# Optimization experiments

Measured on AMD Instinct MI355X. Metric: run time of the kernel, lower is better.

Reference implementation:

```python
import jax, jax.numpy as jnp
import numpy as np

B, N, CHUNK, LAH = 2, 16, 60, 4
EXT = CHUNK + LAH            # extended chunk size C+R
S = N * EXT                  # flattened (chunked) time dim
D, FF, H, K, L = 512, 2048, 8, 31, 6
DH = D // H
EPS = 1e-5


def _ln(x, g, b):
    m = x.mean(-1, keepdims=True)
    v = ((x - m) ** 2).mean(-1, keepdims=True)
    return (x - m) * jax.lax.rsqrt(v + EPS) * g + b


def _chunk_mask(lookahead_size):
    # True = query may attend key. Queries see all past chunks (excluding the
    # carried-over lookahead frames of past chunks) plus the full current
    # extended chunk (its own real frames and its own lookahead frames).
    idx = jnp.arange(S)
    c = idx // EXT           # chunk index of each flattened position
    w = idx % EXT            # position within extended chunk
    past = (c[None, :] < c[:, None]) & (w[None, :] < EXT - lookahead_size)
    curr = c[None, :] == c[:, None]
    return past | curr       # [S, S]


def setup_inputs():
    key = jax.random.key(0)
    ks = iter(jax.random.split(key, 16))

    def pr(shape, s=0.02):
        return jax.random.normal(next(ks), (L,) + shape, jnp.float32) * s

    ones = lambda shape: jnp.ones((L,) + shape, jnp.float32)
    zeros = lambda shape: jnp.zeros((L,) + shape, jnp.float32)
    return dict(
        x=jax.random.normal(next(ks), (B, N, EXT, D), jnp.float32),
        sequence_mask=jnp.ones((B, N, EXT), bool).at[:, -1, CHUNK - 10:].set(False),
        lookahead_size=LAH,
        ff1_lng=ones((D,)), ff1_lnb=zeros((D,)),
        ff1_w1=pr((D, FF)), ff1_b1=zeros((FF,)),
        ff1_w2=pr((FF, D)), ff1_b2=zeros((D,)),
        att_lng=ones((D,)), att_lnb=zeros((D,)),
        wqkv=pr((D, 3 * D)), bqkv=zeros((3 * D,)),
        wo=pr((D, D)), bo=zeros((D,)),
        conv_lng=ones((D,)), conv_lnb=zeros((D,)),
        pw1_w=pr((D, 2 * D)), pw1_b=zeros((2 * D,)),
        dw_w=pr((K, 1, D)), dw_b=zeros((D,)),
        cn_g=ones((D,)), cn_b=zeros((D,)),
        pw2_w=pr((D, D)), pw2_b=zeros((D,)),
        ff2_lng=ones((D,)), ff2_lnb=zeros((D,)),
        ff2_w1=pr((D, FF)), ff2_b1=zeros((FF,)),
        ff2_w2=pr((FF, D)), ff2_b2=zeros((D,)),
        fin_g=ones((D,)), fin_b=zeros((D,)),
    )


def _forward(x, sequence_mask, lookahead_size,
             ff1_lng, ff1_lnb, ff1_w1, ff1_b1, ff1_w2, ff1_b2,
             att_lng, att_lnb, wqkv, bqkv, wo, bo,
             conv_lng, conv_lnb, pw1_w, pw1_b, dw_w, dw_b, cn_g, cn_b, pw2_w, pw2_b,
             ff2_lng, ff2_lnb, ff2_w1, ff2_b1, ff2_w2, ff2_b2, fin_g, fin_b):
    xf = x.reshape(B, S, D)
    key_valid = sequence_mask.reshape(B, S)
    allowed = _chunk_mask(lookahead_size)[None, None] & key_valid[:, None, None, :]  # [B,1,S,S]
    scale = 1.0 / np.sqrt(DH).astype(np.float32)

    def ff(h, lng, lnb, w1, b1, w2, b2):
        h = _ln(h, lng, lnb)
        h = jax.nn.silu(h @ w1 + b1)
        return h @ w2 + b2

    def block(h, pr):
        (f1g, f1b, f1w1, f1b1, f1w2, f1b2,
         alg, alb, wq, bq, wo_, bo_,
         clg, clb, p1w, p1b, dww, dwb, cng, cnb, p2w, p2b,
         f2g, f2b, f2w1, f2b1, f2w2, f2b2, fg, fb) = pr
        # 0.5 * FF1 + residual
        h = 0.5 * ff(h, f1g, f1b, f1w1, f1b1, f1w2, f1b2) + h
        # MHSA with block-diagonal + lookahead chunk mask
        y = _ln(h, alg, alb)
        qkv = y @ wq + bq
        q, k, v = jnp.split(qkv, 3, axis=-1)
        q = q.reshape(B, S, H, DH)
        k = k.reshape(B, S, H, DH)
        v = v.reshape(B, S, H, DH)
        sc = jnp.einsum("bqhd,bkhd->bhqk", q, k) * scale
        sc = jnp.where(allowed, sc, -1e30)
        a = jax.nn.softmax(sc, axis=-1)
        o = jnp.einsum("bhqk,bkhd->bqhd", a, v).reshape(B, S, D)
        h = o @ wo_ + bo_ + h
        # zero padded frames before conv (masked_fill in torch)
        h = jnp.where(key_valid[..., None], h, 0.0)
        # conv module: LN -> pw(2D) -> GLU -> depthwise conv -> LN(NC) -> silu -> pw
        c = _ln(h, clg, clb)
        c = c @ p1w + p1b
        ca, cb = jnp.split(c, 2, axis=-1)
        c = ca * jax.nn.sigmoid(cb)
        c = jax.lax.conv_general_dilated(
            c, dww, window_strides=(1,), padding=[(K // 2, K // 2)],
            dimension_numbers=("NWC", "WIO", "NWC"), feature_group_count=D) + dwb
        c = _ln(c, cng, cnb)
        c = jax.nn.silu(c)
        c = c @ p2w + p2b
        h = c + h
        # 0.5 * FF2 + residual, final LN
        h = 0.5 * ff(h, f2g, f2b, f2w1, f2b1, f2w2, f2b2) + h
        h = _ln(h, fg, fb)
        return h, None

    params = (ff1_lng, ff1_lnb, ff1_w1, ff1_b1, ff1_w2, ff1_b2,
              att_lng, att_lnb, wqkv, bqkv, wo, bo,
              conv_lng, conv_lnb, pw1_w, pw1_b, dw_w, dw_b, cn_g, cn_b, pw2_w, pw2_b,
              ff2_lng, ff2_lnb, ff2_w1, ff2_b1, ff2_w2, ff2_b2, fin_g, fin_b)
    out, _ = jax.lax.scan(block, xf, params)
    # strip lookahead frames: [B, N, C, D]
    return out.reshape(B, N, EXT, D)[:, :, :EXT - lookahead_size]


def reference(x, sequence_mask, lookahead_size,
              ff1_lng, ff1_lnb, ff1_w1, ff1_b1, ff1_w2, ff1_b2,
              att_lng, att_lnb, wqkv, bqkv, wo, bo,
              conv_lng, conv_lnb, pw1_w, pw1_b, dw_w, dw_b, cn_g, cn_b, pw2_w, pw2_b,
              ff2_lng, ff2_lnb, ff2_w1, ff2_b1, ff2_w2, ff2_b2, fin_g, fin_b):
    return _forward(x, sequence_mask, lookahead_size,
                    ff1_lng, ff1_lnb, ff1_w1, ff1_b1, ff1_w2, ff1_b2,
                    att_lng, att_lnb, wqkv, bqkv, wo, bo,
                    conv_lng, conv_lnb, pw1_w, pw1_b, dw_w, dw_b, cn_g, cn_b, pw2_w, pw2_b,
                    ff2_lng, ff2_lnb, ff2_w1, ff2_b1, ff2_w2, ff2_b2, fin_g, fin_b)
```

## Files before the change

### kernel.cpp

```cpp
#include <hip/hip_runtime.h>
#include <hip/hip_bf16.h>
#include <math.h>

#define BB   2
#define NN   16
#define EXTC 64
#define SS   1024
#define DD   512
#define FFD  2048
#define HH   8
#define DHD  64
#define KW   31
#define LL   6
#define BSROWS (BB*SS)
#define LN_EPS 1e-5f

#define EPI_STORE    0
#define EPI_SILU_BF  1
#define EPI_ADD      2
#define EPI_ADDHALF  3
#define EPI_ADD_MASK 4
#define EPI_STORE_BF 5
#define EPI_PART     6

__device__ __forceinline__ int mask_val(const void* m, int i) {
    unsigned int w0 = *(const unsigned int*)m;
    if (w0 == 0x01010101u) return ((const unsigned char*)m)[i];
    if (w0 == 0x3F803F80u) return (((const unsigned short*)m)[i] != 0);
    if (w0 == 0x3F800000u) return (((const float*)m)[i] != 0.0f);
    return (((const int*)m)[i] != 0);
}

__device__ __forceinline__ float sigmoidf_(float x) { return 1.0f / (1.0f + __expf(-x)); }

__device__ __forceinline__ unsigned short f2bf_(float x) {
    unsigned int u = __float_as_uint(x);
    u += 0x7FFF + ((u >> 16) & 1);
    return (unsigned short)(u >> 16);
}

typedef __attribute__((ext_vector_type(8))) short bf16x8;
typedef __attribute__((ext_vector_type(4))) float f32x4;

__global__ __launch_bounds__(256) void ln_kernel(
    const float* __restrict__ in, const float* __restrict__ g,
    const float* __restrict__ b, void* __restrict__ out, int do_silu, int out_bf)
{
    int row = blockIdx.x;
    int t = threadIdx.x;
    const float* ip = in + (size_t)row * DD;
    float v0 = ip[t], v1 = ip[t + 256];
    float s = v0 + v1, ss = v0 * v0 + v1 * v1;
    #pragma unroll
    for (int o = 32; o; o >>= 1) { s += __shfl_down(s, o); ss += __shfl_down(ss, o); }
    __shared__ float sh[8];
    int wid = t >> 6, lane = t & 63;
    if (lane == 0) { sh[wid] = s; sh[4 + wid] = ss; }
    __syncthreads();
    if (t == 0) {
        float S = sh[0] + sh[1] + sh[2] + sh[3];
        float SSum = sh[4] + sh[5] + sh[6] + sh[7];
        float m = S * (1.0f / DD);
        float var = SSum * (1.0f / DD) - m * m;
        sh[0] = m;
        sh[1] = rsqrtf(var + LN_EPS);
    }
    __syncthreads();
    float m = sh[0], rs = sh[1];
    float o0 = (v0 - m) * rs * g[t] + b[t];
    float o1 = (v1 - m) * rs * g[t + 256] + b[t + 256];
    if (do_silu) { o0 = o0 * sigmoidf_(o0); o1 = o1 * sigmoidf_(o1); }
    if (out_bf) {
        unsigned short* op = (unsigned short*)out + (size_t)row * DD;
        op[t] = f2bf_(o0);
        op[t + 256] = f2bf_(o1);
    } else {
        float* op = (float*)out + (size_t)row * DD;
        op[t] = o0;
        op[t + 256] = o1;
    }
}

#define WARENA_LSTRIDE 6029312
__global__ __launch_bounds__(256) void pretrans_kernel(
    const float* __restrict__ w0, const float* __restrict__ w1,
    const float* __restrict__ w2, const float* __restrict__ w3,
    const float* __restrict__ w4, const float* __restrict__ w5,
    const float* __restrict__ w6, const float* __restrict__ w7,
    unsigned short* __restrict__ dst)
{
    const int starts[8] = {0, 256, 512, 704, 768, 896, 960, 1216};
    const int kdim[8]   = {512, 2048, 512, 512, 512, 512, 512, 2048};
    const int ndim[8]   = {2048, 512, 1536, 512, 1024, 512, 2048, 512};
    const int dstoff[8] = {0, 1048576, 2097152, 2883584, 3145728, 3670016, 3932160, 4980736};
    const float* wlist[8] = {w0, w1, w2, w3, w4, w5, w6, w7};
    int layer = blockIdx.y;
    int tile = blockIdx.x;
    int wi = 0;
    #pragma unroll
    for (int i = 7; i >= 1; --i) if (tile >= starts[i]) { wi = i; break; }
    int lt = tile - starts[wi];
    int K = kdim[wi], N = ndim[wi];
    int nT = N >> 6;
    int tk = lt / nT, tn = lt - tk * nT;
    const float* src = wlist[wi] + (size_t)layer * K * N;
    unsigned short* d = dst + (size_t)layer * WARENA_LSTRIDE + dstoff[wi];
    __shared__ float S[64][65];
    int t = threadIdx.x;
    int c = t & 63, r4 = t >> 6;
    #pragma unroll
    for (int u = 0; u < 16; ++u) {
        int row = u * 4 + r4;
        S[row][c] = src[(size_t)(tk * 64 + row) * N + tn * 64 + c];
    }
    __syncthreads();
    #pragma unroll
    for (int u = 0; u < 16; ++u) {
        int nrow = u * 4 + r4;
        d[(size_t)(tn * 64 + nrow) * K + tk * 64 + c] = f2bf_(S[c][nrow]);
    }
}

#define GSTR 72
template<bool WT>
__global__ __launch_bounds__(256) void gemm2_kernel(
    const unsigned short* __restrict__ A, const void* __restrict__ Wv,
    const float* __restrict__ bias, const float* __restrict__ res,
    const void* __restrict__ maskraw,
    float* __restrict__ outf, unsigned short* __restrict__ outb,
    float* __restrict__ part, int M, int N, int Kd, int mode)
{
    __shared__ unsigned short As[64 * GSTR];
    __shared__ unsigned short Bs[64 * GSTR];
    int t = threadIdx.x, lane = t & 63, wave = t >> 6;
    int wr = wave >> 1, wc = wave & 1;
    int l15 = lane & 15, l4 = lane >> 4;
    int row0 = blockIdx.y * 64, col0 = blockIdx.x * 64;
    int kPer = Kd / gridDim.z;
    int k0 = blockIdx.z * kPer;
    int iters = kPer >> 6;
    int ar = t >> 2, ak = (t & 3) * 16;
    int wn = t & 63, wk0 = (t >> 6) * 16;

    f32x4 zero = {0.f, 0.f, 0.f, 0.f};
    f32x4 acc[2][2];
    acc[0][0] = zero; acc[0][1] = zero; acc[1][0] = zero; acc[1][1] = zero;

    uint4 aR0, aR1, wR0, wR1;
    float wF[16];
    {
        const unsigned short* ap = A + (size_t)(row0 + ar) * Kd + k0 + ak;
        aR0 = *(const uint4*)ap; aR1 = *(const uint4*)(ap + 8);
        if constexpr (WT) {
            const unsigned short* wp = (const unsigned short*)Wv + (size_t)(col0 + ar) * Kd + k0 + ak;
            wR0 = *(const uint4*)wp; wR1 = *(const uint4*)(wp + 8);
        } else {
            const float* wp = (const float*)Wv + (size_t)(k0 + wk0) * N + col0 + wn;
            #pragma unroll
            for (int kk = 0; kk < 16; ++kk) wF[kk] = wp[(size_t)kk * N];
        }
    }
    for (int it = 0; it < iters; ++it) {
        __syncthreads();
        *(uint4*)&As[ar * GSTR + ak]     = aR0;
        *(uint4*)&As[ar * GSTR + ak + 8] = aR1;
        if constexpr (WT) {
            *(uint4*)&Bs[ar * GSTR + ak]     = wR0;
            *(uint4*)&Bs[ar * GSTR + ak + 8] = wR1;
        } else {
            union { unsigned short u16[16]; uint4 q[2]; } pk;
            #pragma unroll
            for (int kk = 0; kk < 16; ++kk) pk.u16[kk] = f2bf_(wF[kk]);
            uint4* dstp = (uint4*)&Bs[wn * GSTR + wk0];
            dstp[0] = pk.q[0];
            dstp[1] = pk.q[1];
        }
        __syncthreads();
        if (it + 1 < iters) {
            int kn = k0 + (it + 1) * 64;
            const unsigned short* ap = A + (size_t)(row0 + ar) * Kd + kn + ak;
            aR0 = *(const uint4*)ap; aR1 = *(const uint4*)(ap + 8);
            if constexpr (WT) {
                const unsigned short* wp = (const unsigned short*)Wv + (size_t)(col0 + ar) * Kd + kn + ak;
                wR0 = *(const uint4*)wp; wR1 = *(const uint4*)(wp + 8);
            } else {
                const float* wp = (const float*)Wv + (size_t)(kn + wk0) * N + col0 + wn;
                #pragma unroll
                for (int kk = 0; kk < 16; ++kk) wF[kk] = wp[(size_t)kk * N];
            }
        }
        #pragma unroll
        for (int s = 0; s < 2; ++s) {
            bf16x8 af0 = *(const bf16x8*)&As[(wr * 32 + l15) * GSTR + s * 32 + l4 * 8];
            bf16x8 af1 = *(const bf16x8*)&As[(wr * 32 + 16 + l15) * GSTR + s * 32 + l4 * 8];
            bf16x8 bf0 = *(const bf16x8*)&Bs[(wc * 32 + l15) * GSTR + s * 32 + l4 * 8];
            bf16x8 bf1 = *(const bf16x8*)&Bs[(wc * 32 + 16 + l15) * GSTR + s * 32 + l4 * 8];
            acc[0][0] = __builtin_amdgcn_mfma_f32_16x16x32_bf16(af0, bf0, acc[0][0], 0, 0, 0);
            acc[0][1] = __builtin_amdgcn_mfma_f32_16x16x32_bf16(af0, bf1, acc[0][1], 0, 0, 0);
            acc[1][0] = __builtin_amdgcn_mfma_f32_16x16x32_bf16(af1, bf0, acc[1][0], 0, 0, 0);
            acc[1][1] = __builtin_amdgcn_mfma_f32_16x16x32_bf16(af1, bf1, acc[1][1], 0, 0, 0);
        }
    }
    #pragma unroll
    for (int i = 0; i < 2; i++) {
        #pragma unroll
        for (int j = 0; j < 2; j++) {
            int colb = col0 + wc * 32 + j * 16 + l15;
            #pragma unroll
            for (int r = 0; r < 4; r++) {
                int row = row0 + wr * 32 + i * 16 + l4 * 4 + r;
                size_t off = (size_t)row * N + colb;
                float v = acc[i][j][r];
                if (mode == EPI_PART) { part[(size_t)blockIdx.z * M * N + off] = v; continue; }
                v += bias[colb];
                if (mode == EPI_SILU_BF)       outb[off] = f2bf_(v * sigmoidf_(v));
                else if (mode == EPI_STORE_BF) outb[off] = f2bf_(v);
                else if (mode == EPI_ADD)      outf[off] = v + res[off];
                else if (mode == EPI_ADDHALF)  outf[off] = 0.5f * v + res[off];
                else if (mode == EPI_ADD_MASK) {
                    v = v + res[off];
                    if (!mask_val(maskraw, row)) v = 0.0f;
                    outf[off] = v;
                }
                else                           outf[off] = v;
            }
        }
    }
}

__global__ __launch_bounds__(256) void reduce_addhalf_kernel(
    const float* __restrict__ part, const float* __restrict__ bias,
    float* __restrict__ outAres, int MN, int N)
{
    int idx = (blockIdx.x * 256 + threadIdx.x) * 4;
    float4 p0 = *(const float4*)&part[idx];
    float4 p1 = *(const float4*)&part[MN + idx];
    int col = idx & (N - 1);
    float4 bi = *(const float4*)&bias[col];
    float4 rv = *(const float4*)&outAres[idx];
    float4 o;
    o.x = 0.5f * (p0.x + p1.x + bi.x) + rv.x;
    o.y = 0.5f * (p0.y + p1.y + bi.y) + rv.y;
    o.z = 0.5f * (p0.z + p1.z + bi.z) + rv.z;
    o.w = 0.5f * (p0.w + p1.w + bi.w) + rv.w;
    *(float4*)&outAres[idx] = o;
}

#define QSTR 72
__global__ __launch_bounds__(256) void attn_mfma_kernel(
    const unsigned short* __restrict__ qkv, const void* __restrict__ maskraw,
    const int* __restrict__ lah_ptr, unsigned short* __restrict__ o)
{
    __shared__ unsigned short Qs[64 * QSTR];
    __shared__ unsigned short Ks[64 * QSTR];
    __shared__ unsigned short Vt[64 * QSTR];
    __shared__ unsigned short Ps[64 * QSTR];
    int idx = blockIdx.x;
    int qc = idx & 15;
    int h  = (idx >> 4) & 7;
    int b  = idx >> 7;
    int t  = threadIdx.x;
    int wave = t >> 6, lane = t & 63;
    int l15 = lane & 15, g = lane >> 4;
    int lah = lah_ptr[0];
    int lim = EXTC - lah;
    size_t base = (size_t)b * SS * 3 * DD;
    int ldr = t >> 2;
    int ldc = (t & 3) * 16;

    {
        const unsigned short* gp = qkv + base + (size_t)(qc * 64 + ldr) * (3 * DD) + h * DHD + ldc;
        *(uint4*)&Qs[ldr * QSTR + ldc]     = *(const uint4*)gp;
        *(uint4*)&Qs[ldr * QSTR + ldc + 8] = *(const uint4*)(gp + 8);
    }
    f32x4 accO[4];
    f32x4 zero = {0.f, 0.f, 0.f, 0.f};
    #pragma unroll
    for (int j = 0; j < 4; j++) accO[j] = zero;
    float m[4], l[4];
    #pragma unroll
    for (int r = 0; r < 4; r++) { m[r] = -INFINITY; l[r] = 0.0f; }

    for (int kc = 0; kc <= qc; ++kc) {
        {
            const unsigned short* kp = qkv + base + (size_t)(kc * 64 + ldr) * (3 * DD) + DD + h * DHD + ldc;
            *(uint4*)&Ks[ldr * QSTR + ldc]     = *(const uint4*)kp;
            *(uint4*)&Ks[ldr * QSTR + ldc + 8] = *(const uint4*)(kp + 8);
        }
        {
            const unsigned short* vp = qkv + base + (size_t)(kc * 64 + ldr) * (3 * DD) + 2 * DD + h * DHD + ldc;
            union { uint4 q[2]; unsigned short u16[16]; } vv;
            vv.q[0] = *(const uint4*)vp;
            vv.q[1] = *(const uint4*)(vp + 8);
            #pragma unroll
            for (int u = 0; u < 16; u++)
                Vt[(ldc + u) * QSTR + ldr] = vv.u16[u];
        }
        __syncthreads();
        bf16x8 aq0 = *(const bf16x8*)&Qs[(wave * 16 + l15) * QSTR + g * 8];
        bf16x8 aq1 = *(const bf16x8*)&Qs[(wave * 16 + l15) * QSTR + 32 + g * 8];
        f32x4 sacc[4];
        #pragma unroll
        for (int j = 0; j < 4; j++) {
            bf16x8 bk0 = *(const bf16x8*)&Ks[(j * 16 + l15) * QSTR + g * 8];
            bf16x8 bk1 = *(const bf16x8*)&Ks[(j * 16 + l15) * QSTR + 32 + g * 8];
            sacc[j] = __builtin_amdgcn_mfma_f32_16x16x32_bf16(aq0, bk0, zero, 0, 0, 0);
            sacc[j] = __builtin_amdgcn_mfma_f32_16x16x32_bf16(aq1, bk1, sacc[j], 0, 0, 0);
        }
        bool curr = (kc == qc);
        #pragma unroll
        for (int j = 0; j < 4; ++j) {
            int kpos = j * 16 + l15;
            bool ok = (curr || (kpos < lim)) && (mask_val(maskraw, b * SS + kc * 64 + kpos) != 0);
            #pragma unroll
            for (int r = 0; r < 4; r++)
                sacc[j][r] = ok ? sacc[j][r] * 0.125f : -1e30f;
        }
        #pragma unroll
        for (int r = 0; r < 4; ++r) {
            float rv = fmaxf(fmaxf(sacc[0][r], sacc[1][r]), fmaxf(sacc[2][r], sacc[3][r]));
            rv = fmaxf(rv, __shfl_xor(rv, 1));
            rv = fmaxf(rv, __shfl_xor(rv, 2));
            rv = fmaxf(rv, __shfl_xor(rv, 4));
            rv = fmaxf(rv, __shfl_xor(rv, 8));
            float mn = fmaxf(m[r], rv);
            float alpha = __expf(m[r] - mn);
            float p0 = __expf(sacc[0][r] - mn), p1 = __expf(sacc[1][r] - mn);
            float p2 = __expf(sacc[2][r] - mn), p3 = __expf(sacc[3][r] - mn);
            float ps = p0 + p1 + p2 + p3;
            ps += __shfl_xor(ps, 1);
            ps += __shfl_xor(ps, 2);
            ps += __shfl_xor(ps, 4);
            ps += __shfl_xor(ps, 8);
            l[r] = l[r] * alpha + ps;
            m[r] = mn;
            #pragma unroll
            for (int j = 0; j < 4; j++) accO[j][r] *= alpha;
            int qrow = wave * 16 + g * 4 + r;
            Ps[qrow * QSTR +  0 + l15] = f2bf_(p0);
            Ps[qrow * QSTR + 16 + l15] = f2bf_(p1);
            Ps[qrow * QSTR + 32 + l15] = f2bf_(p2);
            Ps[qrow * QSTR + 48 + l15] = f2bf_(p3);
        }
        __syncthreads();
        bf16x8 ap0 = *(const bf16x8*)&Ps[(wave * 16 + l15) * QSTR + g * 8];
        bf16x8 ap1 = *(const bf16x8*)&Ps[(wave * 16 + l15) * QSTR + 32 + g * 8];
        #pragma unroll
        for (int j = 0; j < 4; j++) {
            bf16x8 bv0 = *(const bf16x8*)&Vt[(j * 16 + l15) * QSTR + g * 8];
            bf16x8 bv1 = *(const bf16x8*)&Vt[(j * 16 + l15) * QSTR + 32 + g * 8];
            accO[j] = __builtin_amdgcn_mfma_f32_16x16x32_bf16(ap0, bv0, accO[j], 0, 0, 0);
            accO[j] = __builtin_amdgcn_mfma_f32_16x16x32_bf16(ap1, bv1, accO[j], 0, 0, 0);
        }
        __syncthreads();
    }
    #pragma unroll
    for (int r = 0; r < 4; r++) {
        float inv = 1.0f / l[r];
        size_t row = (size_t)b * SS + qc * 64 + wave * 16 + g * 4 + r;
        #pragma unroll
        for (int j = 0; j < 4; j++)
            o[row * DD + h * DHD + j * 16 + l15] = f2bf_(accO[j][r] * inv);
    }
}

__global__ __launch_bounds__(256) void glu_kernel(
    const float* __restrict__ in, float* __restrict__ out)
{
    int idx = blockIdx.x * 256 + threadIdx.x;
    int d4 = (idx & 127) * 4;
    int r = idx >> 7;
    float4 a = *(const float4*)&in[(size_t)r * 2 * DD + d4];
    float4 gt = *(const float4*)&in[(size_t)r * 2 * DD + DD + d4];
    float4 res;
    res.x = a.x * sigmoidf_(gt.x);
    res.y = a.y * sigmoidf_(gt.y);
    res.z = a.z * sigmoidf_(gt.z);
    res.w = a.w * sigmoidf_(gt.w);
    *(float4*)&out[(size_t)idx * 4] = res;
}

__global__ __launch_bounds__(256) void dwconv_ln_silu_kernel(
    const float* __restrict__ in, const float* __restrict__ w,
    const float* __restrict__ bias, const float* __restrict__ g,
    const float* __restrict__ be, unsigned short* __restrict__ out)
{
    int t = threadIdx.x;
    int half = t >> 7;
    int row = blockIdx.x * 2 + half;
    int d4 = (t & 127) * 4;
    int s = row & (SS - 1), b = row >> 10;
    float4 acc = *(const float4*)&bias[d4];
    #pragma unroll
    for (int k = 0; k < KW; k++) {
        int sp = s + k - KW / 2;
        if (sp >= 0 && sp < SS) {
            float4 x = *(const float4*)&in[((size_t)b * SS + sp) * DD + d4];
            float4 ww = *(const float4*)&w[k * DD + d4];
            acc.x = fmaf(x.x, ww.x, acc.x);
            acc.y = fmaf(x.y, ww.y, acc.y);
            acc.z = fmaf(x.z, ww.z, acc.z);
            acc.w = fmaf(x.w, ww.w, acc.w);
        }
    }
    float sm = acc.x + acc.y + acc.z + acc.w;
    float sq = acc.x * acc.x + acc.y * acc.y + acc.z * acc.z + acc.w * acc.w;
    #pragma unroll
    for (int o = 32; o; o >>= 1) { sm += __shfl_down(sm, o); sq += __shfl_down(sq, o); }
    __shared__ float sh[8];
    int wid = t >> 6, lane = t & 63;
    if (lane == 0) { sh[wid] = sm; sh[4 + wid] = sq; }
    __syncthreads();
    float S = sh[half * 2] + sh[half * 2 + 1];
    float Q = sh[4 + half * 2] + sh[4 + half * 2 + 1];
    float mean = S * (1.0f / DD);
    float rs = rsqrtf(Q * (1.0f / DD) - mean * mean + LN_EPS);
    float4 gg = *(const float4*)&g[d4];
    float4 bb = *(const float4*)&be[d4];
    float y0 = (acc.x - mean) * rs * gg.x + bb.x;
    float y1 = (acc.y - mean) * rs * gg.y + bb.y;
    float y2 = (acc.z - mean) * rs * gg.z + bb.z;
    float y3 = (acc.w - mean) * rs * gg.w + bb.w;
    y0 *= sigmoidf_(y0); y1 *= sigmoidf_(y1); y2 *= sigmoidf_(y2); y3 *= sigmoidf_(y3);
    uint2 pk;
    pk.x = (unsigned int)f2bf_(y0) | ((unsigned int)f2bf_(y1) << 16);
    pk.y = (unsigned int)f2bf_(y2) | ((unsigned int)f2bf_(y3) << 16);
    *(uint2*)&out[(size_t)row * DD + d4] = pk;
}

__global__ __launch_bounds__(256) void store_out_kernel(
    const float* __restrict__ hbuf, float* __restrict__ out)
{
    int idx = blockIdx.x * 256 + threadIdx.x;
    int d = idx & (DD - 1);
    int rest = idx >> 9;
    int c = rest % 60;
    int bn = rest / 60;
    out[idx] = hbuf[((size_t)bn * EXTC + c) * DD + d];
}

extern "C" void kernel_launch(void* const* d_in, const int* in_sizes, int n_in,
                              void* d_out, int out_size, void* d_ws, size_t ws_size,
                              hipStream_t stream)
{
    const float* x    = (const float*)d_in[0];
    const void*  mask = d_in[1];
    const int*   lah  = (const int*)d_in[2];
    #define P(i) ((const float*)d_in[i])

    char* wsb = (char*)d_ws;
    float*          A   = (float*)(wsb);
    unsigned short* Ybf = (unsigned short*)(wsb + (4u<<20));
    char*           U   = wsb + (6u<<20);
    float*          Db  = (float*)(wsb + (18u<<20));
    unsigned short* Dbf = (unsigned short*)(wsb + (22u<<20));
    float*          Part = (float*)(wsb + (18u<<20));
    float*          Uf  = (float*)U;
    unsigned short* Ub  = (unsigned short*)U;
    unsigned short* Wt  = (unsigned short*)(wsb + (26u<<20));
    bool wt = ws_size >= (100ull << 20);

    hipMemcpyAsync(A, x, (size_t)BSROWS * DD * 4, hipMemcpyDeviceToDevice, stream);
    if (wt) {
        dim3 gpt(1472, LL);
        pretrans_kernel<<<gpt, 256, 0, stream>>>(P(5), P(7), P(11), P(13), P(17),
                                                 P(23), P(27), P(29), Wt);
    }
    const size_t woff[8] = {0, 1048576, 2097152, 2883584, 3145728, 3670016, 3932160, 4980736};

    #define GEMM(grid, Aptr, Wfp, wi, bias, res, mk, of, ob, pt, M_, N_, K_, md)            \
        do { if (wt)                                                                         \
            gemm2_kernel<true><<<grid, 256, 0, stream>>>(Aptr,                               \
                (const void*)(Wt + (size_t)l * WARENA_LSTRIDE + woff[wi]), bias, res, mk,    \
                of, ob, pt, M_, N_, K_, md);                                                 \
        else                                                                                 \
            gemm2_kernel<false><<<grid, 256, 0, stream>>>(Aptr, (const void*)(Wfp), bias,    \
                res, mk, of, ob, pt, M_, N_, K_, md); } while (0)

    dim3 gFF1 (FFD / 64,    BSROWS / 64, 1);
    dim3 gW2  (DD / 64,     BSROWS / 64, 2);
    dim3 gQKV (3 * DD / 64, BSROWS / 64, 1);
    dim3 gP1  (2 * DD / 64, BSROWS / 64, 1);
    dim3 gDx  (DD / 64,     BSROWS / 64, 1);
    int ew4_blocks = BSROWS * DD / 4 / 256;

    for (int l = 0; l < LL; l++) {
        const float* f1g  = P(3)  + (size_t)l * DD;
        const float* f1b  = P(4)  + (size_t)l * DD;
        const float* f1w1 = P(5)  + (size_t)l * DD * FFD;
        const float* f1b1 = P(6)  + (size_t)l * FFD;
        const float* f1w2 = P(7)  + (size_t)l * FFD * DD;
        const float* f1b2 = P(8)  + (size_t)l * DD;
        const float* alg  = P(9)  + (size_t)l * DD;
        const float* alb  = P(10) + (size_t)l * DD;
        const float* wqkv = P(11) + (size_t)l * DD * 3 * DD;
        const float* bqkv = P(12) + (size_t)l * 3 * DD;
        const float* wo   = P(13) + (size_t)l * DD * DD;
        const float* bo   = P(14) + (size_t)l * DD;
        const float* clg  = P(15) + (size_t)l * DD;
        const float* clb  = P(16) + (size_t)l * DD;
        const float* p1w  = P(17) + (size_t)l * DD * 2 * DD;
        const float* p1b  = P(18) + (size_t)l * 2 * DD;
        const float* dww  = P(19) + (size_t)l * KW * DD;
        const float* dwb  = P(20) + (size_t)l * DD;
        const float* cng  = P(21) + (size_t)l * DD;
        const float* cnb  = P(22) + (size_t)l * DD;
        const float* p2w  = P(23) + (size_t)l * DD * DD;
        const float* p2b  = P(24) + (size_t)l * DD;
        const float* f2g  = P(25) + (size_t)l * DD;
        const float* f2b  = P(26) + (size_t)l * DD;
        const float* f2w1 = P(27) + (size_t)l * DD * FFD;
        const float* f2b1 = P(28) + (size_t)l * FFD;
        const float* f2w2 = P(29) + (size_t)l * FFD * DD;
        const float* f2b2 = P(30) + (size_t)l * DD;
        const float* fing = P(31) + (size_t)l * DD;
        const float* finb = P(32) + (size_t)l * DD;

        ln_kernel<<<BSROWS, 256, 0, stream>>>(A, f1g, f1b, Ybf, 0, 1);
        GEMM(gFF1, Ybf, f1w1, 0, f1b1, nullptr, nullptr, nullptr, Ub, nullptr,
             BSROWS, FFD, DD, EPI_SILU_BF);
        GEMM(gW2, Ub, f1w2, 1, nullptr, nullptr, nullptr, nullptr, nullptr, Part,
             BSROWS, DD, FFD, EPI_PART);
        reduce_addhalf_kernel<<<BSROWS * DD / 1024, 256, 0, stream>>>(Part, f1b2, A,
             BSROWS * DD, DD);

        ln_kernel<<<BSROWS, 256, 0, stream>>>(A, alg, alb, Ybf, 0, 1);
        GEMM(gQKV, Ybf, wqkv, 2, bqkv, nullptr, nullptr, nullptr, Ub, nullptr,
             BSROWS, 3 * DD, DD, EPI_STORE_BF);
        attn_mfma_kernel<<<BB * HH * NN, 256, 0, stream>>>(Ub, mask, lah, Dbf);
        GEMM(gDx, Dbf, wo, 3, bo, A, mask, A, nullptr, nullptr,
             BSROWS, DD, DD, EPI_ADD_MASK);

        ln_kernel<<<BSROWS, 256, 0, stream>>>(A, clg, clb, Ybf, 0, 1);
        GEMM(gP1, Ybf, p1w, 4, p1b, nullptr, nullptr, Uf, nullptr, nullptr,
             BSROWS, 2 * DD, DD, EPI_STORE);
        glu_kernel<<<ew4_blocks, 256, 0, stream>>>(Uf, Db);
        dwconv_ln_silu_kernel<<<BSROWS / 2, 256, 0, stream>>>(Db, dww, dwb, cng, cnb, Ybf);
        GEMM(gDx, Ybf, p2w, 5, p2b, A, nullptr, A, nullptr, nullptr,
             BSROWS, DD, DD, EPI_ADD);

        ln_kernel<<<BSROWS, 256, 0, stream>>>(A, f2g, f2b, Ybf, 0, 1);
        GEMM(gFF1, Ybf, f2w1, 6, f2b1, nullptr, nullptr, nullptr, Ub, nullptr,
             BSROWS, FFD, DD, EPI_SILU_BF);
        GEMM(gW2, Ub, f2w2, 7, nullptr, nullptr, nullptr, nullptr, nullptr, Part,
             BSROWS, DD, FFD, EPI_PART);
        reduce_addhalf_kernel<<<BSROWS * DD / 1024, 256, 0, stream>>>(Part, f2b2, A,
             BSROWS * DD, DD);

        ln_kernel<<<BSROWS, 256, 0, stream>>>(A, fing, finb, A, 0, 0);
    }

    store_out_kernel<<<(BB * NN * 60 * DD) / 256, 256, 0, stream>>>(A, (float*)d_out);
    #undef GEMM
    #undef P
}
```

Before: 1.477 ms.

## Fuse split-K reduce with layernorms, fuse pointwise GEMM with GLU, bf16 intermediates

Merges the split-K reduction of each FFN second GEMM with the following layernorm (and, for FFN2, with the final LN, the next layer's first LN and the output strip). Fuses the first conv pointwise GEMM with the GLU gating so it writes bf16 directly and skips the fp32 intermediate. The conv path now stores the GLU output in bf16. Also vectorizes the pretranspose stores and drops the initial memcpy and the separate store kernel. This cuts launches and memory traffic, at the cost of slightly lower precision in the conv intermediate.

```diff
diff --git a/kernel.cpp b/kernel.cpp
--- a/kernel.cpp
+++ b/kernel.cpp
@@ -18,7 +18,6 @@
 #define EPI_STORE    0
 #define EPI_SILU_BF  1
 #define EPI_ADD      2
-#define EPI_ADDHALF  3
 #define EPI_ADD_MASK 4
 #define EPI_STORE_BF 5
 #define EPI_PART     6
@@ -38,13 +37,16 @@
     u += 0x7FFF + ((u >> 16) & 1);
     return (unsigned short)(u >> 16);
 }
+__device__ __forceinline__ float bf2f_(unsigned short b) {
+    return __uint_as_float(((unsigned int)b) << 16);
+}
 
 typedef __attribute__((ext_vector_type(8))) short bf16x8;
 typedef __attribute__((ext_vector_type(4))) float f32x4;
 
 __global__ __launch_bounds__(256) void ln_kernel(
     const float* __restrict__ in, const float* __restrict__ g,
-    const float* __restrict__ b, void* __restrict__ out, int do_silu, int out_bf)
+    const float* __restrict__ b, unsigned short* __restrict__ out)
 {
     int row = blockIdx.x;
     int t = threadIdx.x;
@@ -57,28 +59,91 @@
     int wid = t >> 6, lane = t & 63;
     if (lane == 0) { sh[wid] = s; sh[4 + wid] = ss; }
     __syncthreads();
-    if (t == 0) {
-        float S = sh[0] + sh[1] + sh[2] + sh[3];
-        float SSum = sh[4] + sh[5] + sh[6] + sh[7];
-        float m = S * (1.0f / DD);
-        float var = SSum * (1.0f / DD) - m * m;
-        sh[0] = m;
-        sh[1] = rsqrtf(var + LN_EPS);
-    }
+    float S = sh[0] + sh[1] + sh[2] + sh[3];
+    float Q = sh[4] + sh[5] + sh[6] + sh[7];
+    float m = S * (1.0f / DD);
+    float rs = rsqrtf(Q * (1.0f / DD) - m * m + LN_EPS);
+    out[(size_t)row * DD + t]       = f2bf_((v0 - m) * rs * g[t] + b[t]);
+    out[(size_t)row * DD + t + 256] = f2bf_((v1 - m) * rs * g[t + 256] + b[t + 256]);
+}
+
+__global__ __launch_bounds__(256) void reduce_ln_kernel(
+    const float* __restrict__ part, const float* __restrict__ bias,
+    const float* __restrict__ res, float* __restrict__ A,
+    const float* __restrict__ g, const float* __restrict__ b,
+    unsigned short* __restrict__ Ybf)
+{
+    int row = blockIdx.x, t = threadIdx.x;
+    size_t o0 = (size_t)row * DD + t, o1 = o0 + 256;
+    const int MN = BSROWS * DD;
+    float h0 = 0.5f * (part[o0] + part[MN + o0] + bias[t])       + res[o0];
+    float h1 = 0.5f * (part[o1] + part[MN + o1] + bias[t + 256]) + res[o1];
+    A[o0] = h0; A[o1] = h1;
+    float s = h0 + h1, ss = h0 * h0 + h1 * h1;
+    #pragma unroll
+    for (int o = 32; o; o >>= 1) { s += __shfl_down(s, o); ss += __shfl_down(ss, o); }
+    __shared__ float sh[8];
+    int wid = t >> 6, lane = t & 63;
+    if (lane == 0) { sh[wid] = s; sh[4 + wid] = ss; }
     __syncthreads();
-    float m = sh[0], rs = sh[1];
-    float o0 = (v0 - m) * rs * g[t] + b[t];
-    float o1 = (v1 - m) * rs * g[t + 256] + b[t + 256];
-    if (do_silu) { o0 = o0 * sigmoidf_(o0); o1 = o1 * sigmoidf_(o1); }
-    if (out_bf) {
-        unsigned short* op = (unsigned short*)out + (size_t)row * DD;
-        op[t] = f2bf_(o0);
-        op[t + 256] = f2bf_(o1);
-    } else {
-        float* op = (float*)out + (size_t)row * DD;
-        op[t] = o0;
-        op[t + 256] = o1;
-    }
+    float S = sh[0] + sh[1] + sh[2] + sh[3];
+    float Q = sh[4] + sh[5] + sh[6] + sh[7];
+    float m = S * (1.0f / DD);
+    float rs = rsqrtf(Q * (1.0f / DD) - m * m + LN_EPS);
+    Ybf[o0] = f2bf_((h0 - m) * rs * g[t] + b[t]);
+    Ybf[o1] = f2bf_((h1 - m) * rs * g[t + 256] + b[t + 256]);
+}
+
+__global__ __launch_bounds__(256) void reduce_lnln_kernel(
+    const float* __restrict__ part, const float* __restrict__ bias,
+    float* __restrict__ A,
+    const float* __restrict__ fing, const float* __restrict__ finb,
+    const float* __restrict__ g2, const float* __restrict__ b2,
+    unsigned short* __restrict__ Ybf, int last, float* __restrict__ outp)
+{
+    int row = blockIdx.x, t = threadIdx.x;
+    size_t o0 = (size_t)row * DD + t, o1 = o0 + 256;
+    const int MN = BSROWS * DD;
+    float h0 = 0.5f * (part[o0] + part[MN + o0] + bias[t])       + A[o0];
+    float h1 = 0.5f * (part[o1] + part[MN + o1] + bias[t + 256]) + A[o1];
+    __shared__ float sh[8];
+    int wid = t >> 6, lane = t & 63;
+    {
+        float s = h0 + h1, ss = h0 * h0 + h1 * h1;
+        #pragma unroll
+        for (int o = 32; o; o >>= 1) { s += __shfl_down(s, o); ss += __shfl_down(ss, o); }
+        if (lane == 0) { sh[wid] = s; sh[4 + wid] = ss; }
+    }
+    __syncthreads();
+    float S = sh[0] + sh[1] + sh[2] + sh[3];
+    float Q = sh[4] + sh[5] + sh[6] + sh[7];
+    float m = S * (1.0f / DD);
+    float rs = rsqrtf(Q * (1.0f / DD) - m * m + LN_EPS);
+    float f0 = (h0 - m) * rs * fing[t] + finb[t];
+    float f1 = (h1 - m) * rs * fing[t + 256] + finb[t + 256];
+    A[o0] = f0; A[o1] = f1;
+    if (last) {
+        int c = row & 63, bn = row >> 6;
+        if (c < 60) {
+            size_t oo = ((size_t)(bn * 60 + c)) * DD + t;
+            outp[oo] = f0; outp[oo + 256] = f1;
+        }
+        return;
+    }
+    __syncthreads();
+    {
+        float s = f0 + f1, ss = f0 * f0 + f1 * f1;
+        #pragma unroll
+        for (int o = 32; o; o >>= 1) { s += __shfl_down(s, o); ss += __shfl_down(ss, o); }
+        if (lane == 0) { sh[wid] = s; sh[4 + wid] = ss; }
+    }
+    __syncthreads();
+    float S2 = sh[0] + sh[1] + sh[2] + sh[3];
+    float Q2 = sh[4] + sh[5] + sh[6] + sh[7];
+    float m2 = S2 * (1.0f / DD);
+    float rs2 = rsqrtf(Q2 * (1.0f / DD) - m2 * m2 + LN_EPS);
+    Ybf[o0] = f2bf_((f0 - m2) * rs2 * g2[t] + b2[t]);
+    Ybf[o1] = f2bf_((f1 - m2) * rs2 * g2[t + 256] + b2[t + 256]);
 }
 
 #define WARENA_LSTRIDE 6029312
@@ -105,19 +170,23 @@
     int tk = lt / nT, tn = lt - tk * nT;
     const float* src = wlist[wi] + (size_t)layer * K * N;
     unsigned short* d = dst + (size_t)layer * WARENA_LSTRIDE + dstoff[wi];
-    __shared__ float S[64][65];
+    __shared__ float Sm[64][65];
     int t = threadIdx.x;
     int c = t & 63, r4 = t >> 6;
     #pragma unroll
     for (int u = 0; u < 16; ++u) {
         int row = u * 4 + r4;
-        S[row][c] = src[(size_t)(tk * 64 + row) * N + tn * 64 + c];
+        Sm[row][c] = src[(size_t)(tk * 64 + row) * N + tn * 64 + c];
     }
     __syncthreads();
     #pragma unroll
-    for (int u = 0; u < 16; ++u) {
-        int nrow = u * 4 + r4;
-        d[(size_t)(tn * 64 + nrow) * K + tk * 64 + c] = f2bf_(S[c][nrow]);
+    for (int p = 0; p < 4; ++p) {
+        int nrow = p * 16 + (t >> 4);
+        int koff = (t & 15) * 4;
+        uint2 pk;
+        pk.x = (unsigned int)f2bf_(Sm[koff + 0][nrow]) | ((unsigned int)f2bf_(Sm[koff + 1][nrow]) << 16);
+        pk.y = (unsigned int)f2bf_(Sm[koff + 2][nrow]) | ((unsigned int)f2bf_(Sm[koff + 3][nrow]) << 16);
+        *(uint2*)&d[(size_t)(tn * 64 + nrow) * K + tk * 64 + koff] = pk;
     }
 }
 
@@ -216,7 +285,6 @@
                 if (mode == EPI_SILU_BF)       outb[off] = f2bf_(v * sigmoidf_(v));
                 else if (mode == EPI_STORE_BF) outb[off] = f2bf_(v);
                 else if (mode == EPI_ADD)      outf[off] = v + res[off];
-                else if (mode == EPI_ADDHALF)  outf[off] = 0.5f * v + res[off];
                 else if (mode == EPI_ADD_MASK) {
                     v = v + res[off];
                     if (!mask_val(maskraw, row)) v = 0.0f;
@@ -228,22 +296,83 @@
     }
 }
 
-__global__ __launch_bounds__(256) void reduce_addhalf_kernel(
-    const float* __restrict__ part, const float* __restrict__ bias,
-    float* __restrict__ outAres, int MN, int N)
-{
-    int idx = (blockIdx.x * 256 + threadIdx.x) * 4;
-    float4 p0 = *(const float4*)&part[idx];
-    float4 p1 = *(const float4*)&part[MN + idx];
-    int col = idx & (N - 1);
-    float4 bi = *(const float4*)&bias[col];
-    float4 rv = *(const float4*)&outAres[idx];
-    float4 o;
-    o.x = 0.5f * (p0.x + p1.x + bi.x) + rv.x;
-    o.y = 0.5f * (p0.y + p1.y + bi.y) + rv.y;
-    o.z = 0.5f * (p0.z + p1.z + bi.z) + rv.z;
-    o.w = 0.5f * (p0.w + p1.w + bi.w) + rv.w;
-    *(float4*)&outAres[idx] = o;
+__global__ __launch_bounds__(256) void gemm_p1glu_kernel(
+    const unsigned short* __restrict__ A, const unsigned short* __restrict__ Wp,
+    const float* __restrict__ p1b, unsigned short* __restrict__ outb)
+{
+    __shared__ unsigned short As[64 * GSTR];
+    __shared__ unsigned short Bs[128 * GSTR];
+    int t = threadIdx.x, lane = t & 63, wave = t >> 6;
+    int wr = wave >> 1, wc = wave & 1;
+    int l15 = lane & 15, l4 = lane >> 4;
+    int row0 = blockIdx.y * 64, g0 = blockIdx.x * 64;
+    int ar = t >> 2, ak = (t & 3) * 16;
+
+    f32x4 zero = {0.f, 0.f, 0.f, 0.f};
+    f32x4 acca[2][2], accg[2][2];
+    acca[0][0] = zero; acca[0][1] = zero; acca[1][0] = zero; acca[1][1] = zero;
+    accg[0][0] = zero; accg[0][1] = zero; accg[1][0] = zero; accg[1][1] = zero;
+
+    uint4 aR0, aR1, bA0, bA1, bG0, bG1;
+    {
+        const unsigned short* ap = A + (size_t)(row0 + ar) * DD + ak;
+        aR0 = *(const uint4*)ap; aR1 = *(const uint4*)(ap + 8);
+        const unsigned short* wa = Wp + (size_t)(g0 + ar) * DD + ak;
+        bA0 = *(const uint4*)wa; bA1 = *(const uint4*)(wa + 8);
+        const unsigned short* wg = Wp + (size_t)(g0 + 512 + ar) * DD + ak;
+        bG0 = *(const uint4*)wg; bG1 = *(const uint4*)(wg + 8);
+    }
+    for (int it = 0; it < 8; ++it) {
+        __syncthreads();
+        *(uint4*)&As[ar * GSTR + ak]            = aR0;
+        *(uint4*)&As[ar * GSTR + ak + 8]        = aR1;
+        *(uint4*)&Bs[ar * GSTR + ak]            = bA0;
+        *(uint4*)&Bs[ar * GSTR + ak + 8]        = bA1;
+        *(uint4*)&Bs[(64 + ar) * GSTR + ak]     = bG0;
+        *(uint4*)&Bs[(64 + ar) * GSTR + ak + 8] = bG1;
+        __syncthreads();
+        if (it + 1 < 8) {
+            int kn = (it + 1) * 64;
+            const unsigned short* ap = A + (size_t)(row0 + ar) * DD + kn + ak;
+            aR0 = *(const uint4*)ap; aR1 = *(const uint4*)(ap + 8);
+            const unsigned short* wa = Wp + (size_t)(g0 + ar) * DD + kn + ak;
+            bA0 = *(const uint4*)wa; bA1 = *(const uint4*)(wa + 8);
+            const unsigned short* wg = Wp + (size_t)(g0 + 512 + ar) * DD + kn + ak;
+            bG0 = *(const uint4*)wg; bG1 = *(const uint4*)(wg + 8);
+        }
+        #pragma unroll
+        for (int s = 0; s < 2; ++s) {
+            bf16x8 af0 = *(const bf16x8*)&As[(wr * 32 + l15) * GSTR + s * 32 + l4 * 8];
+            bf16x8 af1 = *(const bf16x8*)&As[(wr * 32 + 16 + l15) * GSTR + s * 32 + l4 * 8];
+            bf16x8 ba0 = *(const bf16x8*)&Bs[(wc * 32 + l15) * GSTR + s * 32 + l4 * 8];
+            bf16x8 ba1 = *(const bf16x8*)&Bs[(wc * 32 + 16 + l15) * GSTR + s * 32 + l4 * 8];
+            bf16x8 bg0 = *(const bf16x8*)&Bs[(64 + wc * 32 + l15) * GSTR + s * 32 + l4 * 8];
+            bf16x8 bg1 = *(const bf16x8*)&Bs[(64 + wc * 32 + 16 + l15) * GSTR + s * 32 + l4 * 8];
+            acca[0][0] = __builtin_amdgcn_mfma_f32_16x16x32_bf16(af0, ba0, acca[0][0], 0, 0, 0);
+            acca[0][1] = __builtin_amdgcn_mfma_f32_16x16x32_bf16(af0, ba1, acca[0][1], 0, 0, 0);
+            acca[1][0] = __builtin_amdgcn_mfma_f32_16x16x32_bf16(af1, ba0, acca[1][0], 0, 0, 0);
+            acca[1][1] = __builtin_amdgcn_mfma_f32_16x16x32_bf16(af1, ba1, acca[1][1], 0, 0, 0);
+            accg[0][0] = __builtin_amdgcn_mfma_f32_16x16x32_bf16(af0, bg0, accg[0][0], 0, 0, 0);
+            accg[0][1] = __builtin_amdgcn_mfma_f32_16x16x32_bf16(af0, bg1, accg[0][1], 0, 0, 0);
+            accg[1][0] = __builtin_amdgcn_mfma_f32_16x16x32_bf16(af1, bg0, accg[1][0], 0, 0, 0);
+            accg[1][1] = __builtin_amdgcn_mfma_f32_16x16x32_bf16(af1, bg1, accg[1][1], 0, 0, 0);
+        }
+    }
+    #pragma unroll
+    for (int i = 0; i < 2; i++) {
+        #pragma unroll
+        for (int j = 0; j < 2; j++) {
+            int col = g0 + wc * 32 + j * 16 + l15;
+            float ba = p1b[col], bg = p1b[col + 512];
+            #pragma unroll
+            for (int r = 0; r < 4; r++) {
+                int row = row0 + wr * 32 + i * 16 + l4 * 4 + r;
+                float a = acca[i][j][r] + ba;
+                float gt = accg[i][j][r] + bg;
+                outb[(size_t)row * DD + col] = f2bf_(a * sigmoidf_(gt));
+            }
+        }
+    }
 }
 
 #define QSTR 72
@@ -365,23 +494,21 @@
 }
 
 __global__ __launch_bounds__(256) void glu_kernel(
-    const float* __restrict__ in, float* __restrict__ out)
+    const float* __restrict__ in, unsigned short* __restrict__ out)
 {
     int idx = blockIdx.x * 256 + threadIdx.x;
     int d4 = (idx & 127) * 4;
     int r = idx >> 7;
     float4 a = *(const float4*)&in[(size_t)r * 2 * DD + d4];
     float4 gt = *(const float4*)&in[(size_t)r * 2 * DD + DD + d4];
-    float4 res;
-    res.x = a.x * sigmoidf_(gt.x);
-    res.y = a.y * sigmoidf_(gt.y);
-    res.z = a.z * sigmoidf_(gt.z);
-    res.w = a.w * sigmoidf_(gt.w);
-    *(float4*)&out[(size_t)idx * 4] = res;
+    uint2 pk;
+    pk.x = (unsigned int)f2bf_(a.x * sigmoidf_(gt.x)) | ((unsigned int)f2bf_(a.y * sigmoidf_(gt.y)) << 16);
+    pk.y = (unsigned int)f2bf_(a.z * sigmoidf_(gt.z)) | ((unsigned int)f2bf_(a.w * sigmoidf_(gt.w)) << 16);
+    *(uint2*)&out[(size_t)r * DD + d4] = pk;
 }
 
 __global__ __launch_bounds__(256) void dwconv_ln_silu_kernel(
-    const float* __restrict__ in, const float* __restrict__ w,
+    const unsigned short* __restrict__ in, const float* __restrict__ w,
     const float* __restrict__ bias, const float* __restrict__ g,
     const float* __restrict__ be, unsigned short* __restrict__ out)
 {
@@ -395,12 +522,12 @@
     for (int k = 0; k < KW; k++) {
         int sp = s + k - KW / 2;
         if (sp >= 0 && sp < SS) {
-            float4 x = *(const float4*)&in[((size_t)b * SS + sp) * DD + d4];
+            uint2 xv = *(const uint2*)&in[((size_t)b * SS + sp) * DD + d4];
             float4 ww = *(const float4*)&w[k * DD + d4];
-            acc.x = fmaf(x.x, ww.x, acc.x);
-            acc.y = fmaf(x.y, ww.y, acc.y);
-            acc.z = fmaf(x.z, ww.z, acc.z);
-            acc.w = fmaf(x.w, ww.w, acc.w);
+            acc.x = fmaf(bf2f_((unsigned short)(xv.x & 0xFFFF)), ww.x, acc.x);
+            acc.y = fmaf(bf2f_((unsigned short)(xv.x >> 16)),    ww.y, acc.y);
+            acc.z = fmaf(bf2f_((unsigned short)(xv.y & 0xFFFF)), ww.z, acc.z);
+            acc.w = fmaf(bf2f_((unsigned short)(xv.y >> 16)),    ww.w, acc.w);
         }
     }
     float sm = acc.x + acc.y + acc.z + acc.w;
@@ -428,17 +555,6 @@
     *(uint2*)&out[(size_t)row * DD + d4] = pk;
 }
 
-__global__ __launch_bounds__(256) void store_out_kernel(
-    const float* __restrict__ hbuf, float* __restrict__ out)
-{
-    int idx = blockIdx.x * 256 + threadIdx.x;
-    int d = idx & (DD - 1);
-    int rest = idx >> 9;
-    int c = rest % 60;
-    int bn = rest / 60;
-    out[idx] = hbuf[((size_t)bn * EXTC + c) * DD + d];
-}
-
 extern "C" void kernel_launch(void* const* d_in, const int* in_sizes, int n_in,
                               void* d_out, int out_size, void* d_ws, size_t ws_size,
                               hipStream_t stream)
@@ -452,7 +568,7 @@
     float*          A   = (float*)(wsb);
     unsigned short* Ybf = (unsigned short*)(wsb + (4u<<20));
     char*           U   = wsb + (6u<<20);
-    float*          Db  = (float*)(wsb + (18u<<20));
+    unsigned short* Db  = (unsigned short*)(wsb + (18u<<20));
     unsigned short* Dbf = (unsigned short*)(wsb + (22u<<20));
     float*          Part = (float*)(wsb + (18u<<20));
     float*          Uf  = (float*)U;
@@ -460,7 +576,6 @@
     unsigned short* Wt  = (unsigned short*)(wsb + (26u<<20));
     bool wt = ws_size >= (100ull << 20);
 
-    hipMemcpyAsync(A, x, (size_t)BSROWS * DD * 4, hipMemcpyDeviceToDevice, stream);
     if (wt) {
         dim3 gpt(1472, LL);
         pretrans_kernel<<<gpt, 256, 0, stream>>>(P(5), P(7), P(11), P(13), P(17),
@@ -481,8 +596,8 @@
     dim3 gW2  (DD / 64,     BSROWS / 64, 2);
     dim3 gQKV (3 * DD / 64, BSROWS / 64, 1);
     dim3 gP1  (2 * DD / 64, BSROWS / 64, 1);
+    dim3 gGLU (DD / 64,     BSROWS / 64, 1);
     dim3 gDx  (DD / 64,     BSROWS / 64, 1);
-    int ew4_blocks = BSROWS * DD / 4 / 256;
 
     for (int l = 0; l < LL; l++) {
         const float* f1g  = P(3)  + (size_t)l * DD;
@@ -516,41 +631,45 @@
         const float* fing = P(31) + (size_t)l * DD;
         const float* finb = P(32) + (size_t)l * DD;
 
-        ln_kernel<<<BSROWS, 256, 0, stream>>>(A, f1g, f1b, Ybf, 0, 1);
+        if (l == 0)
+            ln_kernel<<<BSROWS, 256, 0, stream>>>(x, f1g, f1b, Ybf);
         GEMM(gFF1, Ybf, f1w1, 0, f1b1, nullptr, nullptr, nullptr, Ub, nullptr,
              BSROWS, FFD, DD, EPI_SILU_BF);
         GEMM(gW2, Ub, f1w2, 1, nullptr, nullptr, nullptr, nullptr, nullptr, Part,
              BSROWS, DD, FFD, EPI_PART);
-        reduce_addhalf_kernel<<<BSROWS * DD / 1024, 256, 0, stream>>>(Part, f1b2, A,
-             BSROWS * DD, DD);
-
-        ln_kernel<<<BSROWS, 256, 0, stream>>>(A, alg, alb, Ybf, 0, 1);
+        reduce_ln_kernel<<<BSROWS, 256, 0, stream>>>(Part, f1b2, (l == 0) ? x : A,
+                                                     A, alg, alb, Ybf);
+
         GEMM(gQKV, Ybf, wqkv, 2, bqkv, nullptr, nullptr, nullptr, Ub, nullptr,
              BSROWS, 3 * DD, DD, EPI_STORE_BF);
         attn_mfma_kernel<<<BB * HH * NN, 256, 0, stream>>>(Ub, mask, lah, Dbf);
         GEMM(gDx, Dbf, wo, 3, bo, A, mask, A, nullptr, nullptr,
              BSROWS, DD, DD, EPI_ADD_MASK);
 
-        ln_kernel<<<BSROWS, 256, 0, stream>>>(A, clg, clb, Ybf, 0, 1);
-        GEMM(gP1, Ybf, p1w, 4, p1b, nullptr, nullptr, Uf, nullptr, nullptr,
-             BSROWS, 2 * DD, DD, EPI_STORE);
-        glu_kernel<<<ew4_blocks, 256, 0, stream>>>(Uf, Db);
+        ln_kernel<<<BSROWS, 256, 0, stream>>>(A, clg, clb, Ybf);
+        if (wt) {
+            gemm_p1glu_kernel<<<gGLU, 256, 0, stream>>>(
+                Ybf, Wt + (size_t)l * WARENA_LSTRIDE + woff[4], p1b, Db);
+        } else {
+            gemm2_kernel<false><<<gP1, 256, 0, stream>>>(Ybf, (const void*)p1w, p1b,
+                nullptr, nullptr, Uf, nullptr, nullptr, BSROWS, 2 * DD, DD, EPI_STORE);
+            glu_kernel<<<BSROWS * DD / 4 / 256, 256, 0, stream>>>(Uf, Db);
+        }
         dwconv_ln_silu_kernel<<<BSROWS / 2, 256, 0, stream>>>(Db, dww, dwb, cng, cnb, Ybf);
         GEMM(gDx, Ybf, p2w, 5, p2b, A, nullptr, A, nullptr, nullptr,
              BSROWS, DD, DD, EPI_ADD);
 
-        ln_kernel<<<BSROWS, 256, 0, stream>>>(A, f2g, f2b, Ybf, 0, 1);
+        ln_kernel<<<BSROWS, 256, 0, stream>>>(A, f2g, f2b, Ybf);
         GEMM(gFF1, Ybf, f2w1, 6, f2b1, nullptr, nullptr, nullptr, Ub, nullptr,
              BSROWS, FFD, DD, EPI_SILU_BF);
         GEMM(gW2, Ub, f2w2, 7, nullptr, nullptr, nullptr, nullptr, nullptr, Part,
              BSROWS, DD, FFD, EPI_PART);
-        reduce_addhalf_kernel<<<BSROWS * DD / 1024, 256, 0, stream>>>(Part, f2b2, A,
-             BSROWS * DD, DD);
-
-        ln_kernel<<<BSROWS, 256, 0, stream>>>(A, fing, finb, A, 0, 0);
-    }
-
-    store_out_kernel<<<(BB * NN * 60 * DD) / 256, 256, 0, stream>>>(A, (float*)d_out);
+        int last = (l == LL - 1);
+        reduce_lnln_kernel<<<BSROWS, 256, 0, stream>>>(Part, f2b2, A, fing, finb,
+            last ? fing : (P(3) + (size_t)(l + 1) * DD),
+            last ? finb : (P(4) + (size_t)(l + 1) * DD),
+            Ybf, last, (float*)d_out);
+    }
     #undef GEMM
     #undef P
 }
```

New measurement: 1.367 ms. 1.08x faster.
